# Optimization experiments

Hardware: AMD Instinct MI355X
Metric: run time of the kernel (lower is better)

The kernel has to match this reference:

```python
import jax, jax.numpy as jnp
import numpy as np

TEMPERATURE = 0.5
N, K, L, D = 2048, 8, 64, 64


def setup_inputs() -> dict:
    key = jax.random.key(0)
    k1, k2, k3 = jax.random.split(key, 3)
    similarity_matrix = jax.random.normal(k1, (N, N), dtype=jnp.float32)
    batch_emb_om = jax.random.normal(k2, (N, L, D), dtype=jnp.float32)
    index = jax.random.randint(k3, (N, K), 0, N, dtype=jnp.int64)
    return {"similarity_matrix": similarity_matrix,
            "batch_emb_om": batch_emb_om,
            "index": index}


def reference(similarity_matrix, batch_emb_om, index):
    # divide=True path of AggregationRebuild
    sim = similarity_matrix / TEMPERATURE
    # gather each row's neighbor similarities: [N, K]
    sub_similarity = jnp.take_along_axis(sim, index, axis=1)
    rebuild_weight_matrix = jax.nn.softmax(sub_similarity, axis=-1)  # [N, K]
    # gather neighbor features: [N, K, L, D]
    neighbor_features = batch_emb_om[index]
    # softmax-weighted sum over neighbors -> [N, L, D]
    rebuild_oral_batch_emb = jnp.einsum('nk,nkld->nld',
                                        rebuild_weight_matrix, neighbor_features)
    return (rebuild_weight_matrix, rebuild_oral_batch_emb)
```

## Files before the change

### kernel.cpp

```cpp
#include <hip/hip_runtime.h>


typedef float f32x4 __attribute__((ext_vector_type(4)));

constexpr int N  = 2048;
constexpr int K  = 8;
constexpr int LD = 64 * 64;
constexpr float INV_TEMP = 2.0f;

constexpr int TILE   = 512;
constexpr int NTILES = LD / TILE;
constexpr int RPB    = 8;

__global__ __launch_bounds__(256) void agg_rebuild_fused(
    const float* __restrict__ sim,
    const float* __restrict__ emb,
    const int*   __restrict__ idx32,
    float* __restrict__ w_out,
    float* __restrict__ rebuild) {
  const int tile = blockIdx.x & (NTILES - 1);
  const int rg   = blockIdx.x >> 3;
  const int r0   = rg * RPB;
  const int tid  = threadIdx.x;

  __shared__ float w_lds[RPB][K];
  __shared__ int   j_lds[RPB][K];
  __shared__ int   is64_s;

  if (tid == 0) {
    int acc = idx32[1] | idx32[3] | idx32[5] | idx32[7] |
              idx32[9] | idx32[11] | idx32[13] | idx32[15];
    is64_s = (acc == 0) ? 1 : 0;
  }
  __syncthreads();

  if (tid < RPB * K) {
    const int rl = tid >> 3;
    const int k  = tid & 7;
    const int flat = (r0 + rl) * K + k;
    const int j = is64_s ? idx32[2 * flat] : idx32[flat];
    const float s =
        __builtin_nontemporal_load(sim + (size_t)(r0 + rl) * N + j) * INV_TEMP;

    float m = s;
    m = fmaxf(m, __shfl_xor(m, 1, 8));
    m = fmaxf(m, __shfl_xor(m, 2, 8));
    m = fmaxf(m, __shfl_xor(m, 4, 8));
    const float e = expf(s - m);
    float sum = e;
    sum += __shfl_xor(sum, 1, 8);
    sum += __shfl_xor(sum, 2, 8);
    sum += __shfl_xor(sum, 4, 8);
    const float w = e / sum;

    w_lds[rl][k] = w;
    j_lds[rl][k] = j;
    if (tile == 0) w_out[flat] = w;
  }
  __syncthreads();

  const int c   = tid & 127;
  const int sub = tid >> 7;
  const int col = tile * TILE + c * 4;

#pragma unroll
  for (int it = 0; it < RPB / 2; ++it) {
    const int rl = it * 2 + sub;
    float w[K];
    const f32x4* p[K];
#pragma unroll
    for (int k = 0; k < K; ++k) {
      w[k] = w_lds[rl][k];
      p[k] = reinterpret_cast<const f32x4*>(emb + (size_t)j_lds[rl][k] * LD + col);
    }
    f32x4 acc = (f32x4)(0.0f);
#pragma unroll
    for (int k = 0; k < K; ++k) {
      const f32x4 v = *p[k];
      acc += w[k] * v;
    }
    f32x4* o = reinterpret_cast<f32x4*>(rebuild + (size_t)(r0 + rl) * LD + col);
    __builtin_nontemporal_store(acc, o);
  }
}

extern "C" void kernel_launch(void* const* d_in, const int* in_sizes, int n_in,
                              void* d_out, int out_size, void* d_ws, size_t ws_size,
                              hipStream_t stream) {
  const float* sim = (const float*)d_in[0];
  const float* emb = (const float*)d_in[1];
  const int*   idx = (const int*)d_in[2];
  float* out     = (float*)d_out;
  float* w_out   = out;
  float* rebuild = out + (size_t)N * K;

  hipLaunchKernelGGL(agg_rebuild_fused, dim3((N / RPB) * NTILES), dim3(256),
                     0, stream, sim, emb, idx, w_out, rebuild);
}
```

Measured before the change: 100.5 us.

## Repack embeddings into tile-major workspace before the gather-weighted sum

Adds a pre-pass kernel that copies the embedding tensor into a tile-major layout in the workspace, so each column tile of all rows is contiguous. The main kernel then gathers neighbor rows from that tile slice, aiming for better cache and TLB locality, since each block touches only one 4 MB slice. The cost is an extra full read and write of the 32 MB embedding tensor on every call, plus a second kernel launch.

```diff
diff --git a/kernel.cpp b/kernel.cpp
--- a/kernel.cpp
+++ b/kernel.cpp
@@ -12,15 +12,33 @@
 constexpr int NTILES = LD / TILE;
 constexpr int RPB    = 8;
 
+__global__ __launch_bounds__(256) void repack_kernel(
+    const float* __restrict__ emb,
+    float* __restrict__ emb_t) {
+  const int t   = blockIdx.x & (NTILES - 1);
+  const int r0  = (blockIdx.x >> 3) * RPB;
+  const int tid = threadIdx.x;
+
+#pragma unroll
+  for (int i = 0; i < RPB * (TILE / 4) / 256; ++i) {
+    const int flat = i * 256 + tid;
+    const int rl = flat >> 7;
+    const int c  = flat & 127;
+    const f32x4 v = *reinterpret_cast<const f32x4*>(
+        emb + (size_t)(r0 + rl) * LD + t * TILE + c * 4);
+    *reinterpret_cast<f32x4*>(
+        emb_t + ((size_t)t * N + (r0 + rl)) * TILE + c * 4) = v;
+  }
+}
+
 __global__ __launch_bounds__(256) void agg_rebuild_fused(
     const float* __restrict__ sim,
-    const float* __restrict__ emb,
+    const float* __restrict__ emb_t,
     const int*   __restrict__ idx32,
     float* __restrict__ w_out,
     float* __restrict__ rebuild) {
   const int tile = blockIdx.x & (NTILES - 1);
-  const int rg   = blockIdx.x >> 3;
-  const int r0   = rg * RPB;
+  const int r0   = (blockIdx.x >> 3) * RPB;
   const int tid  = threadIdx.x;
 
   __shared__ float w_lds[RPB][K];
@@ -61,7 +79,7 @@
 
   const int c   = tid & 127;
   const int sub = tid >> 7;
-  const int col = tile * TILE + c * 4;
+  const float* slice = emb_t + (size_t)tile * N * TILE;
 
 #pragma unroll
   for (int it = 0; it < RPB / 2; ++it) {
@@ -71,7 +89,8 @@
 #pragma unroll
     for (int k = 0; k < K; ++k) {
       w[k] = w_lds[rl][k];
-      p[k] = reinterpret_cast<const f32x4*>(emb + (size_t)j_lds[rl][k] * LD + col);
+      p[k] = reinterpret_cast<const f32x4*>(
+          slice + (size_t)j_lds[rl][k] * TILE + c * 4);
     }
     f32x4 acc = (f32x4)(0.0f);
 #pragma unroll
@@ -79,7 +98,8 @@
       const f32x4 v = *p[k];
       acc += w[k] * v;
     }
-    f32x4* o = reinterpret_cast<f32x4*>(rebuild + (size_t)(r0 + rl) * LD + col);
+    f32x4* o = reinterpret_cast<f32x4*>(
+        rebuild + (size_t)(r0 + rl) * LD + tile * TILE + c * 4);
     __builtin_nontemporal_store(acc, o);
   }
 }
@@ -93,7 +113,10 @@
   float* out     = (float*)d_out;
   float* w_out   = out;
   float* rebuild = out + (size_t)N * K;
+  float* emb_t   = (float*)d_ws;
 
+  hipLaunchKernelGGL(repack_kernel, dim3((N / RPB) * NTILES), dim3(256),
+                     0, stream, emb, emb_t);
   hipLaunchKernelGGL(agg_rebuild_fused, dim3((N / RPB) * NTILES), dim3(256),
-                     0, stream, sim, emb, idx, w_out, rebuild);
+                     0, stream, sim, emb_t, idx, w_out, rebuild);
 }
```

Measured after the change: 111.2 us. 10.7% more time.
